# Kernel tuning notes

Hardware: AMD Instinct MI355X
Metric: run time of the kernel (lower is better)

## Reference

```python
import jax, jax.numpy as jnp
import numpy as np

DIM = 1024
HEADS = 16
HEAD_DIM = DIM // HEADS
EPS = 1e-5
THETA = 10000.0


def _rope(t):
    # t: (b, s, d). lucidrains rotary: interleaved pairs, full-dim rotation, theta=10000.
    b, s, d = t.shape
    inv_freq = 1.0 / (THETA ** (jnp.arange(0, d, 2, dtype=jnp.float32) / d))  # (d/2,)
    ang = jnp.arange(s, dtype=jnp.float32)[:, None] * inv_freq[None, :]        # (s, d/2)
    cos, sin = jnp.cos(ang), jnp.sin(ang)
    tp = t.reshape(b, s, d // 2, 2)
    x1, x2 = tp[..., 0], tp[..., 1]
    o1 = x1 * cos - x2 * sin
    o2 = x2 * cos + x1 * sin
    return jnp.stack([o1, o2], axis=-1).reshape(b, s, d)


def setup_inputs() -> dict:
    key = jax.random.key(0)
    ks = jax.random.split(key, 10)
    b, s, d = 2, 2048, DIM
    scale = 1.0 / np.sqrt(d)
    return {
        "x": jax.random.normal(ks[0], (b, s, d), dtype=jnp.float32),
        "mask": jax.random.normal(ks[1], (b, s, s), dtype=jnp.float32),
        "ln_g": jnp.ones((d,), dtype=jnp.float32),
        "ln_b": jnp.zeros((d,), dtype=jnp.float32),
        "w_qkv": jax.random.normal(ks[2], (3 * d, d), dtype=jnp.float32) * scale,
        "b_qkv": jnp.zeros((3 * d,), dtype=jnp.float32),
        "in_w": jax.random.normal(ks[3], (3 * d, d), dtype=jnp.float32) * scale,
        "in_b": jnp.zeros((3 * d,), dtype=jnp.float32),
        "out_w": jax.random.normal(ks[4], (d, d), dtype=jnp.float32) * scale,
        "out_b": jnp.zeros((d,), dtype=jnp.float32),
    }


def reference(x, mask, ln_g, ln_b, w_qkv, b_qkv, in_w, in_b, out_w, out_b):
    b, s, d = x.shape
    # LayerNorm
    mu = jnp.mean(x, axis=-1, keepdims=True)
    var = jnp.mean((x - mu) ** 2, axis=-1, keepdims=True)
    xn = (x - mu) * jax.lax.rsqrt(var + EPS) * ln_g + ln_b
    # fused qkv projection, then chunk
    qkv = xn @ w_qkv.T + b_qkv
    q, k, v = jnp.split(qkv, 3, axis=-1)
    # RoPE on q, k (full dim, interleaved pairs)
    q = _rope(q)
    k = _rope(k)
    # nn.MultiheadAttention re-applies its own in-projection
    wq, wk, wv = jnp.split(in_w, 3, axis=0)
    bq, bk, bv = jnp.split(in_b, 3, axis=0)
    def to_heads(t, w, bias):
        t = t @ w.T + bias
        return t.reshape(b, s, HEADS, HEAD_DIM).transpose(0, 2, 1, 3)  # (b,h,s,hd)
    qh = to_heads(q, wq, bq)
    kh = to_heads(k, wk, bk)
    vh = to_heads(v, wv, bv)
    scores = jnp.einsum('bhid,bhjd->bhij', qh, kh) / np.sqrt(HEAD_DIM)
    scores = scores + mask[:, None, :, :]  # mask repeated over heads
    attn = jax.nn.softmax(scores, axis=-1)
    out = jnp.einsum('bhij,bhjd->bhid', attn, vh)
    out = out.transpose(0, 2, 1, 3).reshape(b, s, d)
    return out @ out_w.T + out_b
```

## Files before the change

kernel.cpp:

```cpp
#include <hip/hip_runtime.h>

using u16 = unsigned short;
using u32 = unsigned int;
typedef __attribute__((ext_vector_type(8))) short short8;
typedef __attribute__((ext_vector_type(4))) float f32x4;

#define LOG2E 1.4426950408889634f
#define SCALE2 0.18033688011112042f

__device__ __forceinline__ u16 f2b(float f) {
  union { float f; unsigned u; } v; v.f = f;
  unsigned r = v.u + 0x7fffu + ((v.u >> 16) & 1u);
  return (u16)(r >> 16);
}

__device__ __forceinline__ void wg_barrier() {
  asm volatile("s_waitcnt lgkmcnt(0)\n\ts_barrier" ::: "memory");
}

__device__ __forceinline__ void wbar0() {
  asm volatile("s_waitcnt vmcnt(0) lgkmcnt(0)\n\ts_barrier" ::: "memory");
}

__device__ __forceinline__ void gload_lds16(const void* g, void* l) {
  __builtin_amdgcn_global_load_lds(
      (const __attribute__((address_space(1))) unsigned int*)g,
      (__attribute__((address_space(3))) unsigned int*)l, 16, 0, 0);
}

__global__ __launch_bounds__(256) void prep(const float* __restrict__ w_qkv, u16* __restrict__ wqkv_b,
                                            const float* __restrict__ in_w, u16* __restrict__ inw_b,
                                            const float* __restrict__ out_w, u16* __restrict__ outw_b,
                                            float2* __restrict__ rtab,
                                            const float* __restrict__ mask, u16* __restrict__ maskp,
                                            const float* __restrict__ x,
                                            const float* __restrict__ ln_g,
                                            const float* __restrict__ ln_b,
                                            u16* __restrict__ xn) {
  __shared__ u16 T[128 * 68];
  __shared__ float sbuf[4], ssbuf[4];
  int blk = blockIdx.x, t = threadIdx.x;
  if (blk < 7168) {
    int i = blk * 256 + t;
    const float* s; u16* d; int off;
    if (i < 786432)       { s = w_qkv; d = wqkv_b; off = i; }
    else if (i < 1572864) { s = in_w;  d = inw_b;  off = i - 786432; }
    else                  { s = out_w; d = outw_b; off = i - 1572864; }
    float4 v = ((const float4*)s)[off];
    uint2 o;
    o.x = (unsigned)f2b(v.x) | ((unsigned)f2b(v.y) << 16);
    o.y = (unsigned)f2b(v.z) | ((unsigned)f2b(v.w) << 16);
    ((uint2*)d)[off] = o;
  } else if (blk < 11264) {
    int idx = (blk - 7168) * 256 + t;
    int pos = idx >> 9, i = idx & 511;
    float ifreq = exp2f(-(float)(2 * i) * (13.287712379549449f / 1024.0f));
    float ang = (float)pos * ifreq;
    rtab[idx] = make_float2(__cosf(ang), __sinf(ang));
  } else if (blk < 12288) {
    int mb = blk - 11264;
    int kt = mb & 31, qt = (mb >> 5) & 15, bb = mb >> 9;
    const float* src = mask + ((size_t)bb * 2048 + qt * 128) * 2048 + kt * 64;
    #pragma unroll
    for (int it = 0; it < 8; it++) {
      int id = it * 256 + t;
      int r = id >> 4, c4 = (id & 15) * 4;
      float4 v = *(const float4*)(src + (size_t)r * 2048 + c4);
      T[r * 68 + c4 + 0] = f2b(v.x * LOG2E);
      T[r * 68 + c4 + 1] = f2b(v.y * LOG2E);
      T[r * 68 + c4 + 2] = f2b(v.z * LOG2E);
      T[r * 68 + c4 + 3] = f2b(v.w * LOG2E);
    }
    __syncthreads();
    size_t obase = (size_t)(((bb * 16 + qt) * 32) + kt) * 8192;
    #pragma unroll
    for (int it = 0; it < 2; it++) {
      int pos = it * 256 + t;
      int l15 = pos & 15, g = pos >> 4;
      int w = g >> 3, p = (g >> 2) & 1, qd = g & 3;
      int qlocal = w * 32 + p * 16 + l15;
      u16 vals[16];
      #pragma unroll
      for (int mt = 0; mt < 4; mt++)
        #pragma unroll
        for (int reg = 0; reg < 4; reg++)
          vals[mt * 4 + reg] = T[qlocal * 68 + mt * 16 + qd * 4 + reg];
      uint4* dst = (uint4*)(maskp + obase + (size_t)pos * 16);
      dst[0] = *(uint4*)&vals[0];
      dst[1] = *(uint4*)&vals[8];
    }
  } else {
    int row = blk - 12288;
    const float* xr = x + (size_t)row * 1024;
    float4 v = *(const float4*)(xr + t * 4);
    float s = v.x + v.y + v.z + v.w;
    float ss = v.x * v.x + v.y * v.y + v.z * v.z + v.w * v.w;
    #pragma unroll
    for (int m = 1; m < 64; m <<= 1) {
      s  += __shfl_xor(s, m);
      ss += __shfl_xor(ss, m);
    }
    int wave = t >> 6, lane = t & 63;
    if (lane == 0) { sbuf[wave] = s; ssbuf[wave] = ss; }
    __syncthreads();
    s  = sbuf[0] + sbuf[1] + sbuf[2] + sbuf[3];
    ss = ssbuf[0] + ssbuf[1] + ssbuf[2] + ssbuf[3];
    float mean = s * (1.0f / 1024.0f);
    float var  = ss * (1.0f / 1024.0f) - mean * mean;
    float rstd = 1.0f / sqrtf(var + 1e-5f);
    float4 gv = *(const float4*)(ln_g + t * 4);
    float4 bv = *(const float4*)(ln_b + t * 4);
    uint2 o;
    o.x = (unsigned)f2b((v.x - mean) * rstd * gv.x + bv.x) |
          ((unsigned)f2b((v.y - mean) * rstd * gv.y + bv.y) << 16);
    o.y = (unsigned)f2b((v.z - mean) * rstd * gv.z + bv.z) |
          ((unsigned)f2b((v.w - mean) * rstd * gv.w + bv.w) << 16);
    *(uint2*)(xn + (size_t)row * 1024 + t * 4) = o;
  }
}

template<bool SLAB, bool OUT_BF16, bool ROPE, bool WVT>
__global__ __launch_bounds__(256, 3) void gemm_pipe(const u16* __restrict__ A, int lda,
                                                    const u16* __restrict__ W,
                                                    const float* __restrict__ bias,
                                                    const float2* __restrict__ rtab,
                                                    float* __restrict__ Cf,
                                                    u16* __restrict__ Cb,
                                                    u16* __restrict__ vT,
                                                    int ldc, int K) {
  __shared__ u16 As[3][128 * 32];
  __shared__ u16 Bs[3][128 * 32];
  int n0 = blockIdx.x * 128, m0 = blockIdx.y * 128;
  int aoff = SLAB ? ((n0 >> 10) << 10) : 0;
  int tid = threadIdx.x;
  int lane = tid & 63, l15 = lane & 15, quad = lane >> 4;
  int w = tid >> 6, mw = w & 1, nw = w >> 1;
  const u16* Abase = A + (size_t)m0 * lda + aoff;
  const u16* Wbase = W + (size_t)n0 * K;
  f32x4 acc[4][4];
  #pragma unroll
  for (int i = 0; i < 4; i++)
    #pragma unroll
    for (int j = 0; j < 4; j++) acc[i][j] = (f32x4){0.f, 0.f, 0.f, 0.f};

  int rl = lane >> 2;
  int qs = ((lane & 3) ^ ((lane >> 3) & 3)) * 16;
  const char* gA0 = (const char*)(Abase + (size_t)(w * 16 + rl) * lda) + qs;
  const char* gA1 = (const char*)(Abase + (size_t)((w + 4) * 16 + rl) * lda) + qs;
  const char* gB0 = (const char*)(Wbase + (size_t)(w * 16 + rl) * K) + qs;
  const char* gB1 = (const char*)(Wbase + (size_t)((w + 4) * 16 + rl) * K) + qs;
  int p16 = (quad ^ ((l15 >> 1) & 3)) * 8;

  #define ISSUE(bf)                                                           \
    gload_lds16(gA0, &As[bf][(w) * 512]);                                     \
    gload_lds16(gA1, &As[bf][(w + 4) * 512]);                                 \
    gload_lds16(gB0, &Bs[bf][(w) * 512]);                                     \
    gload_lds16(gB1, &Bs[bf][(w + 4) * 512]);                                 \
    gA0 += 64; gA1 += 64; gB0 += 64; gB1 += 64;
  #define WBAR4() asm volatile("s_waitcnt vmcnt(4) lgkmcnt(0)\n\ts_barrier" ::: "memory")
  #define WBAR0() asm volatile("s_waitcnt vmcnt(0) lgkmcnt(0)\n\ts_barrier" ::: "memory")
  #define COMPUTE(bf)                                                         \
    {                                                                         \
      short8 af[4], bfr[4];                                                   \
      _Pragma("unroll")                                                       \
      for (int mt = 0; mt < 4; mt++)                                          \
        af[mt] = *(const short8*)&As[bf][(mw * 64 + mt * 16 + l15) * 32 + p16]; \
      _Pragma("unroll")                                                       \
      for (int nt = 0; nt < 4; nt++)                                          \
        bfr[nt] = *(const short8*)&Bs[bf][(nw * 64 + nt * 16 + l15) * 32 + p16]; \
      _Pragma("unroll")                                                       \
      for (int mt = 0; mt < 4; mt++)                                          \
        _Pragma("unroll")                                                     \
        for (int nt = 0; nt < 4; nt++)                                        \
          acc[mt][nt] = __builtin_amdgcn_mfma_f32_16x16x32_bf16(              \
              af[mt], bfr[nt], acc[mt][nt], 0, 0, 0);                         \
    }

  ISSUE(0);
  ISSUE(1);
  WBAR4();
  #pragma unroll 1
  for (int tt = 0; tt < 10; ++tt) {
    ISSUE(2); COMPUTE(0); WBAR4();
    ISSUE(0); COMPUTE(1); WBAR4();
    ISSUE(1); COMPUTE(2); WBAR4();
  }
  COMPUTE(0); WBAR0();
  COMPUTE(1);
  #undef ISSUE
  #undef WBAR4
  #undef WBAR0
  #undef COMPUTE

  int mb = m0 + mw * 64, nb = n0 + nw * 64;
  float bv[4];
  #pragma unroll
  for (int nt = 0; nt < 4; nt++) bv[nt] = bias[nb + nt * 16 + l15];
  #pragma unroll
  for (int mt = 0; mt < 4; mt++)
    #pragma unroll
    for (int nt = 0; nt < 4; nt++) {
      int col = nb + nt * 16 + l15;
      if (WVT && col >= 2048) {
        int hh = (col - 2048) >> 6, dd = (col - 2048) & 63;
        int row0 = mb + mt * 16 + quad * 4;
        int bbi = row0 >> 11, s0 = row0 & 2047;
        u16 vv[4];
        #pragma unroll
        for (int reg = 0; reg < 4; reg++) vv[reg] = f2b(acc[mt][nt][reg] + bv[nt]);
        *(uint2*)&vT[((size_t)((bbi * 16 + hh) * 64 + dd)) * 2048 + s0] = *(uint2*)vv;
      } else {
        #pragma unroll
        for (int reg = 0; reg < 4; reg++) {
          int row = mb + mt * 16 + quad * 4 + reg;
          float val = acc[mt][nt][reg] + bv[nt];
          if (ROPE && col < 2048) {
            float pr = __shfl_xor(val, 1);
            float2 cs = rtab[(size_t)(row & 2047) * 512 + ((col & 1023) >> 1)];
            val = (col & 1) ? fmaf(val, cs.x, pr * cs.y)
                            : fmaf(val, cs.x, -pr * cs.y);
          }
          if (OUT_BF16) Cb[(size_t)row * ldc + col] = f2b(val);
          else          Cf[(size_t)row * ldc + col] = val;
        }
      }
    }
}

#define SWZ(row, chunk) (((row) << 6) + ((((chunk) ^ ((row) & 7))) << 3))
__global__ __launch_bounds__(512, 4) void attn_mfma(const u16* __restrict__ qkv2,
                                                    const u16* __restrict__ vT,
                                                    const u16* __restrict__ maskp,
                                                    u16* __restrict__ attn_out) {
  __shared__ u16 Kb[2][64 * 64];
  __shared__ u16 Vb[2][64 * 64];
  __shared__ u16 Ps[128 * 72];
  __shared__ float lsf[128];
  int h = blockIdx.x, qt = blockIdx.y, bb = blockIdx.z;
  int tid = threadIdx.x;
  int lane = tid & 63, l15 = lane & 15, quad = lane >> 4;
  int w = tid >> 6;
  int wq = w & 3, wk = w >> 2;
  const u16* kslab = qkv2 + ((size_t)bb * 2048) * 3072 + 1024 + h * 64;
  const u16* vslab = vT + ((size_t)((bb * 16 + h) * 64)) * 2048;

  int drow = lane >> 3, dchunk = (lane & 7) ^ (lane >> 3);
  const u16* kdma = kslab + (size_t)(w * 8 + drow) * 3072 + dchunk * 8;
  const u16* vdma = vslab + (size_t)(w * 8 + drow) * 2048 + dchunk * 8;

  {
    int r = tid >> 2, c0 = (tid & 3) * 16;
    const u16* src = qkv2 + (size_t)(bb * 2048 + qt * 128 + r) * 3072 + h * 64 + c0;
    *(uint4*)&Ps[r * 72 + c0]     = *(const uint4*)src;
    *(uint4*)&Ps[r * 72 + c0 + 8] = *(const uint4*)(src + 8);
  }
  gload_lds16(kdma, &Kb[0][w * 512]);
  gload_lds16(vdma, &Vb[0][w * 512]);
  const u16* mbase = maskp + ((size_t)((bb * 16 + qt) * 32)) * 8192
                     + ((wq * 8 + quad) * 16 + l15) * 16 + wk * 8;
  uint4 m0 = *(const uint4*)mbase;
  uint4 m1 = *(const uint4*)(mbase + 1024);
  wbar0();

  short8 bq[2][2];
  #pragma unroll
  for (int p = 0; p < 2; p++)
    #pragma unroll
    for (int hk = 0; hk < 2; hk++)
      bq[p][hk] = *(const short8*)&Ps[(wq * 32 + p * 16 + l15) * 72 + hk * 32 + quad * 8];
  float lsum[2] = {0.f, 0.f};
  f32x4 acc[2][4];
  #pragma unroll
  for (int p = 0; p < 2; p++)
    #pragma unroll
    for (int dt = 0; dt < 4; dt++) acc[p][dt] = (f32x4){0.f, 0.f, 0.f, 0.f};

  for (int kt = 0; kt < 32; kt++) {
    int b = kt & 1;
    uint4 m0n, m1n;
    if (kt + 1 < 32) {
      gload_lds16(kdma + (size_t)(kt + 1) * 196608, &Kb[b ^ 1][w * 512]);
      gload_lds16(vdma + (size_t)(kt + 1) * 64,     &Vb[b ^ 1][w * 512]);
      m0n = *(const uint4*)(mbase + (size_t)(kt + 1) * 8192);
      m1n = *(const uint4*)(mbase + (size_t)(kt + 1) * 8192 + 1024);
    }
    short8 ak[2][2];
    #pragma unroll
    for (int mt = 0; mt < 2; mt++)
      #pragma unroll
      for (int hk = 0; hk < 2; hk++)
        ak[mt][hk] = *(const short8*)&Kb[b][SWZ(wk * 32 + mt * 16 + l15, hk * 4 + quad)];
    f32x4 st[2][2];
    __builtin_amdgcn_s_setprio(1);
    #pragma unroll
    for (int p = 0; p < 2; p++)
      #pragma unroll
      for (int mt = 0; mt < 2; mt++) {
        f32x4 z = (f32x4){0.f, 0.f, 0.f, 0.f};
        z = __builtin_amdgcn_mfma_f32_16x16x32_bf16(ak[mt][0], bq[p][0], z, 0, 0, 0);
        st[p][mt] = __builtin_amdgcn_mfma_f32_16x16x32_bf16(ak[mt][1], bq[p][1], z, 0, 0, 0);
      }
    __builtin_amdgcn_s_setprio(0);
    #pragma unroll
    for (int p = 0; p < 2; p++) {
      uint4 mm = p ? m1 : m0;
      u32 wds[4] = {mm.x, mm.y, mm.z, mm.w};
      float mv[8];
      #pragma unroll
      for (int j = 0; j < 4; j++) {
        mv[2 * j]     = __uint_as_float(wds[j] << 16);
        mv[2 * j + 1] = __uint_as_float(wds[j] & 0xffff0000u);
      }
      int prow = (wq * 32 + p * 16 + l15) * 72 + wk * 32 + quad * 4;
      #pragma unroll
      for (int mt = 0; mt < 2; mt++) {
        float sv0 = fmaf(st[p][mt][0], SCALE2, mv[mt * 4 + 0]);
        float sv1 = fmaf(st[p][mt][1], SCALE2, mv[mt * 4 + 1]);
        float sv2 = fmaf(st[p][mt][2], SCALE2, mv[mt * 4 + 2]);
        float sv3 = fmaf(st[p][mt][3], SCALE2, mv[mt * 4 + 3]);
        float p0 = __builtin_amdgcn_exp2f(sv0), p1 = __builtin_amdgcn_exp2f(sv1);
        float p2 = __builtin_amdgcn_exp2f(sv2), p3 = __builtin_amdgcn_exp2f(sv3);
        lsum[p] += (p0 + p1) + (p2 + p3);
        u32 pk0, pk1;
        asm("v_cvt_pk_bf16_f32 %0, %1, %2" : "=v"(pk0) : "v"(p0), "v"(p1));
        asm("v_cvt_pk_bf16_f32 %0, %1, %2" : "=v"(pk1) : "v"(p2), "v"(p3));
        *(uint2*)&Ps[prow + mt * 16] = make_uint2(pk0, pk1);
      }
    }
    short8 ap[2];
    #pragma unroll
    for (int p = 0; p < 2; p++)
      ap[p] = *(const short8*)&Ps[(wq * 32 + p * 16 + l15) * 72 + wk * 32 + quad * 8];
    __builtin_amdgcn_s_setprio(1);
    #pragma unroll
    for (int dt = 0; dt < 4; dt++) {
      short8 bv = *(const short8*)&Vb[b][SWZ(dt * 16 + l15, wk * 4 + quad)];
      #pragma unroll
      for (int p = 0; p < 2; p++)
        acc[p][dt] = __builtin_amdgcn_mfma_f32_16x16x32_bf16(ap[p], bv, acc[p][dt], 0, 0, 0);
    }
    __builtin_amdgcn_s_setprio(0);
    if (kt + 1 < 32) { m0 = m0n; m1 = m1n; }
    wbar0();
  }

  float* fs = (wq == 0) ? (float*)&Kb[0][0]
            : (wq == 1) ? (float*)&Vb[0][0]
                        : (float*)&Ps[0] + (wq & 1) * 2176;
  if (wk) {
    #pragma unroll
    for (int p = 0; p < 2; p++) {
      #pragma unroll
      for (int dt = 0; dt < 4; dt++)
        #pragma unroll
        for (int reg = 0; reg < 4; reg++)
          fs[(p * 16 + quad * 4 + reg) * 68 + dt * 16 + l15] = acc[p][dt][reg];
      float l = lsum[p];
      l += __shfl_xor(l, 16);
      l += __shfl_xor(l, 32);
      if (lane < 16) lsf[(wq * 2 + p) * 16 + l15] = l;
    }
  }
  wg_barrier();
  if (!wk) {
    #pragma unroll
    for (int p = 0; p < 2; p++) {
      float l = lsum[p];
      l += __shfl_xor(l, 16);
      l += __shfl_xor(l, 32);
      l += lsf[(wq * 2 + p) * 16 + l15];
      #pragma unroll
      for (int reg = 0; reg < 4; reg++) {
        float lq = __shfl(l, quad * 4 + reg);
        float inv = 1.0f / lq;
        int grow = bb * 2048 + qt * 128 + wq * 32 + p * 16 + quad * 4 + reg;
        #pragma unroll
        for (int dt = 0; dt < 4; dt++) {
          float o = acc[p][dt][reg] + fs[(p * 16 + quad * 4 + reg) * 68 + dt * 16 + l15];
          attn_out[(size_t)grow * 1024 + h * 64 + dt * 16 + l15] = f2b(o * inv);
        }
      }
    }
  }
}

extern "C" void kernel_launch(void* const* d_in, const int* in_sizes, int n_in,
                              void* d_out, int out_size, void* d_ws, size_t ws_size,
                              hipStream_t stream) {
  const float* x     = (const float*)d_in[0];
  const float* mask  = (const float*)d_in[1];
  const float* ln_g  = (const float*)d_in[2];
  const float* ln_b  = (const float*)d_in[3];
  const float* w_qkv = (const float*)d_in[4];
  const float* b_qkv = (const float*)d_in[5];
  const float* in_w  = (const float*)d_in[6];
  const float* in_b  = (const float*)d_in[7];
  const float* out_w = (const float*)d_in[8];
  const float* out_b = (const float*)d_in[9];
  float* out = (float*)d_out;
  char* ws = (char*)d_ws;

  u16* wqkv_b = (u16*)(ws);
  u16* inw_b  = (u16*)(ws + 6291456ull);
  u16* outw_b = (u16*)(ws + 12582912ull);
  u16* xn_b   = (u16*)(ws + 14680064ull);
  u16* attn_b = xn_b;
  u16* qkv_b  = (u16*)(ws + 23068672ull);
  u16* qkv2_b = (u16*)(ws + 48234496ull);
  float2* rtab = (float2*)qkv2_b;
  u16* vT     = (u16*)(ws + 73400320ull);
  u16* maskp  = (u16*)(ws + 81788928ull);

  prep<<<16384, 256, 0, stream>>>(w_qkv, wqkv_b, in_w, inw_b, out_w, outw_b,
                                  rtab, mask, maskp, x, ln_g, ln_b, xn_b);
  gemm_pipe<false, true, true, false><<<dim3(24, 32), 256, 0, stream>>>(
      xn_b, 1024, wqkv_b, b_qkv, rtab, nullptr, qkv_b, nullptr, 3072, 1024);
  gemm_pipe<true, true, false, true><<<dim3(24, 32), 256, 0, stream>>>(
      qkv_b, 3072, inw_b, in_b, nullptr, nullptr, qkv2_b, vT, 3072, 1024);
  attn_mfma<<<dim3(16, 16, 2), 512, 0, stream>>>(qkv2_b, vT, maskp, attn_b);
  gemm_pipe<false, false, false, false><<<dim3(8, 32), 256, 0, stream>>>(
      attn_b, 1024, outw_b, out_b, nullptr, out, nullptr, nullptr, 1024, 1024);
}
```

Measured before the change: 290.1 us.

## Triple-buffer K/V tiles in attention with prefetch distance two

```diff
diff --git a/kernel.cpp b/kernel.cpp
--- a/kernel.cpp
+++ b/kernel.cpp
@@ -20,6 +20,10 @@
 
 __device__ __forceinline__ void wbar0() {
   asm volatile("s_waitcnt vmcnt(0) lgkmcnt(0)\n\ts_barrier" ::: "memory");
+}
+
+__device__ __forceinline__ void cbar2() {
+  asm volatile("s_waitcnt vmcnt(2) lgkmcnt(0)\n\ts_barrier" ::: "memory");
 }
 
 __device__ __forceinline__ void gload_lds16(const void* g, void* l) {
@@ -232,8 +236,8 @@
                                                     const u16* __restrict__ vT,
                                                     const u16* __restrict__ maskp,
                                                     u16* __restrict__ attn_out) {
-  __shared__ u16 Kb[2][64 * 64];
-  __shared__ u16 Vb[2][64 * 64];
+  __shared__ u16 Kb[3][64 * 64];
+  __shared__ u16 Vb[3][64 * 64];
   __shared__ u16 Ps[128 * 72];
   __shared__ float lsf[128];
   int h = blockIdx.x, qt = blockIdx.y, bb = blockIdx.z;
@@ -254,12 +258,14 @@
     *(uint4*)&Ps[r * 72 + c0]     = *(const uint4*)src;
     *(uint4*)&Ps[r * 72 + c0 + 8] = *(const uint4*)(src + 8);
   }
-  gload_lds16(kdma, &Kb[0][w * 512]);
-  gload_lds16(vdma, &Vb[0][w * 512]);
   const u16* mbase = maskp + ((size_t)((bb * 16 + qt) * 32)) * 8192
                      + ((wq * 8 + quad) * 16 + l15) * 16 + wk * 8;
   uint4 m0 = *(const uint4*)mbase;
   uint4 m1 = *(const uint4*)(mbase + 1024);
+  gload_lds16(kdma, &Kb[0][w * 512]);
+  gload_lds16(vdma, &Vb[0][w * 512]);
+  gload_lds16(kdma + 196608, &Kb[1][w * 512]);
+  gload_lds16(vdma + 64,     &Vb[1][w * 512]);
   wbar0();
 
   short8 bq[2][2];
@@ -275,74 +281,86 @@
     #pragma unroll
     for (int dt = 0; dt < 4; dt++) acc[p][dt] = (f32x4){0.f, 0.f, 0.f, 0.f};
 
-  for (int kt = 0; kt < 32; kt++) {
-    int b = kt & 1;
-    uint4 m0n, m1n;
-    if (kt + 1 < 32) {
-      gload_lds16(kdma + (size_t)(kt + 1) * 196608, &Kb[b ^ 1][w * 512]);
-      gload_lds16(vdma + (size_t)(kt + 1) * 64,     &Vb[b ^ 1][w * 512]);
-      m0n = *(const uint4*)(mbase + (size_t)(kt + 1) * 8192);
-      m1n = *(const uint4*)(mbase + (size_t)(kt + 1) * 8192 + 1024);
-    }
-    short8 ak[2][2];
-    #pragma unroll
-    for (int mt = 0; mt < 2; mt++)
-      #pragma unroll
-      for (int hk = 0; hk < 2; hk++)
-        ak[mt][hk] = *(const short8*)&Kb[b][SWZ(wk * 32 + mt * 16 + l15, hk * 4 + quad)];
-    f32x4 st[2][2];
-    __builtin_amdgcn_s_setprio(1);
-    #pragma unroll
-    for (int p = 0; p < 2; p++)
-      #pragma unroll
-      for (int mt = 0; mt < 2; mt++) {
-        f32x4 z = (f32x4){0.f, 0.f, 0.f, 0.f};
-        z = __builtin_amdgcn_mfma_f32_16x16x32_bf16(ak[mt][0], bq[p][0], z, 0, 0, 0);
-        st[p][mt] = __builtin_amdgcn_mfma_f32_16x16x32_bf16(ak[mt][1], bq[p][1], z, 0, 0, 0);
-      }
-    __builtin_amdgcn_s_setprio(0);
-    #pragma unroll
-    for (int p = 0; p < 2; p++) {
-      uint4 mm = p ? m1 : m0;
-      u32 wds[4] = {mm.x, mm.y, mm.z, mm.w};
-      float mv[8];
-      #pragma unroll
-      for (int j = 0; j < 4; j++) {
-        mv[2 * j]     = __uint_as_float(wds[j] << 16);
-        mv[2 * j + 1] = __uint_as_float(wds[j] & 0xffff0000u);
-      }
-      int prow = (wq * 32 + p * 16 + l15) * 72 + wk * 32 + quad * 4;
-      #pragma unroll
-      for (int mt = 0; mt < 2; mt++) {
-        float sv0 = fmaf(st[p][mt][0], SCALE2, mv[mt * 4 + 0]);
-        float sv1 = fmaf(st[p][mt][1], SCALE2, mv[mt * 4 + 1]);
-        float sv2 = fmaf(st[p][mt][2], SCALE2, mv[mt * 4 + 2]);
-        float sv3 = fmaf(st[p][mt][3], SCALE2, mv[mt * 4 + 3]);
-        float p0 = __builtin_amdgcn_exp2f(sv0), p1 = __builtin_amdgcn_exp2f(sv1);
-        float p2 = __builtin_amdgcn_exp2f(sv2), p3 = __builtin_amdgcn_exp2f(sv3);
-        lsum[p] += (p0 + p1) + (p2 + p3);
-        u32 pk0, pk1;
-        asm("v_cvt_pk_bf16_f32 %0, %1, %2" : "=v"(pk0) : "v"(p0), "v"(p1));
-        asm("v_cvt_pk_bf16_f32 %0, %1, %2" : "=v"(pk1) : "v"(p2), "v"(p3));
-        *(uint2*)&Ps[prow + mt * 16] = make_uint2(pk0, pk1);
-      }
-    }
-    short8 ap[2];
-    #pragma unroll
-    for (int p = 0; p < 2; p++)
-      ap[p] = *(const short8*)&Ps[(wq * 32 + p * 16 + l15) * 72 + wk * 32 + quad * 8];
-    __builtin_amdgcn_s_setprio(1);
-    #pragma unroll
-    for (int dt = 0; dt < 4; dt++) {
-      short8 bv = *(const short8*)&Vb[b][SWZ(dt * 16 + l15, wk * 4 + quad)];
-      #pragma unroll
-      for (int p = 0; p < 2; p++)
-        acc[p][dt] = __builtin_amdgcn_mfma_f32_16x16x32_bf16(ap[p], bv, acc[p][dt], 0, 0, 0);
-    }
-    __builtin_amdgcn_s_setprio(0);
-    if (kt + 1 < 32) { m0 = m0n; m1 = m1n; }
-    wbar0();
-  }
+  #define ABODY(KT, CUR, NXT, DO2)                                            \
+  {                                                                           \
+    uint4 m0n, m1n;                                                           \
+    if ((KT) + 1 < 32) {           \
+      m0n = *(const uint4*)(mbase + (size_t)((KT) + 1) * 8192);               \
+      m1n = *(const uint4*)(mbase + (size_t)((KT) + 1) * 8192 + 1024);        \
+    }                                                                         \
+    if (DO2) {    \
+      gload_lds16(kdma + (size_t)((KT) + 2) * 196608, &Kb[NXT][w * 512]);     \
+      gload_lds16(vdma + (size_t)((KT) + 2) * 64,     &Vb[NXT][w * 512]);     \
+    }                                                                         \
+    short8 ak[2][2];                                                          \
+    _Pragma("unroll")                                                         \
+    for (int mt = 0; mt < 2; mt++)                                            \
+      _Pragma("unroll")                                                       \
+      for (int hk = 0; hk < 2; hk++)                                          \
+        ak[mt][hk] = *(const short8*)&Kb[CUR][SWZ(wk * 32 + mt * 16 + l15, hk * 4 + quad)]; \
+    f32x4 st[2][2];                                                           \
+    __builtin_amdgcn_s_setprio(1);                                            \
+    _Pragma("unroll")                                                         \
+    for (int p = 0; p < 2; p++)                                               \
+      _Pragma("unroll")                                                       \
+      for (int mt = 0; mt < 2; mt++) {                                        \
+        f32x4 z = (f32x4){0.f, 0.f, 0.f, 0.f};                                \
+        z = __builtin_amdgcn_mfma_f32_16x16x32_bf16(ak[mt][0], bq[p][0], z, 0, 0, 0); \
+        st[p][mt] = __builtin_amdgcn_mfma_f32_16x16x32_bf16(ak[mt][1], bq[p][1], z, 0, 0, 0); \
+      }                                                                       \
+    __builtin_amdgcn_s_setprio(0);                                            \
+    _Pragma("unroll")                                                         \
+    for (int p = 0; p < 2; p++) {                                             \
+      uint4 mm = p ? m1 : m0;                                                 \
+      u32 wds[4] = {mm.x, mm.y, mm.z, mm.w};                                  \
+      float mv[8];                                                            \
+      _Pragma("unroll")                                                       \
+      for (int j = 0; j < 4; j++) {                                           \
+        mv[2 * j]     = __uint_as_float(wds[j] << 16);                        \
+        mv[2 * j + 1] = __uint_as_float(wds[j] & 0xffff0000u);                \
+      }                                                                       \
+      int prow = (wq * 32 + p * 16 + l15) * 72 + wk * 32 + quad * 4;          \
+      _Pragma("unroll")                                                       \
+      for (int mt = 0; mt < 2; mt++) {                                        \
+        float sv0 = fmaf(st[p][mt][0], SCALE2, mv[mt * 4 + 0]);               \
+        float sv1 = fmaf(st[p][mt][1], SCALE2, mv[mt * 4 + 1]);               \
+        float sv2 = fmaf(st[p][mt][2], SCALE2, mv[mt * 4 + 2]);               \
+        float sv3 = fmaf(st[p][mt][3], SCALE2, mv[mt * 4 + 3]);               \
+        float p0 = __builtin_amdgcn_exp2f(sv0), p1 = __builtin_amdgcn_exp2f(sv1); \
+        float p2 = __builtin_amdgcn_exp2f(sv2), p3 = __builtin_amdgcn_exp2f(sv3); \
+        lsum[p] += (p0 + p1) + (p2 + p3);                                     \
+        u32 pk0, pk1;                                                         \
+        asm("v_cvt_pk_bf16_f32 %0, %1, %2" : "=v"(pk0) : "v"(p0), "v"(p1));   \
+        asm("v_cvt_pk_bf16_f32 %0, %1, %2" : "=v"(pk1) : "v"(p2), "v"(p3));   \
+        *(uint2*)&Ps[prow + mt * 16] = make_uint2(pk0, pk1);                  \
+      }                                                                       \
+    }                                                                         \
+    short8 ap[2];                                                             \
+    _Pragma("unroll")                                                         \
+    for (int p = 0; p < 2; p++)                                               \
+      ap[p] = *(const short8*)&Ps[(wq * 32 + p * 16 + l15) * 72 + wk * 32 + quad * 8]; \
+    __builtin_amdgcn_s_setprio(1);                                            \
+    _Pragma("unroll")                                                         \
+    for (int dt = 0; dt < 4; dt++) {                                          \
+      short8 bv = *(const short8*)&Vb[CUR][SWZ(dt * 16 + l15, wk * 4 + quad)]; \
+      _Pragma("unroll")                                                       \
+      for (int p = 0; p < 2; p++)                                             \
+        acc[p][dt] = __builtin_amdgcn_mfma_f32_16x16x32_bf16(ap[p], bv, acc[p][dt], 0, 0, 0); \
+    }                                                                         \
+    __builtin_amdgcn_s_setprio(0);                                            \
+    if ((KT) + 1 < 32) { m0 = m0n; m1 = m1n; }                                \
+  }
+
+  #pragma unroll 1
+  for (int tt = 0; tt < 10; ++tt) {
+    int k0 = tt * 3;
+    ABODY(k0,     0, 2, 1); cbar2();
+    ABODY(k0 + 1, 1, 0, 1); cbar2();
+    ABODY(k0 + 2, 2, 1, 1); cbar2();
+  }
+  ABODY(30, 0, 0, 0); cbar2();
+  ABODY(31, 1, 0, 0); wg_barrier();
+  #undef ABODY
 
   float* fs = (wq == 0) ? (float*)&Kb[0][0]
             : (wq == 1) ? (float*)&Vb[0][0]
```

Measured after the change: 291.7 us. About the same (+0.6%).
